# Performance work log

Hardware: AMD Instinct MI355X
Metric: run time of the kernel (lower is better)

The kernel has to match this reference:

```python
import jax, jax.numpy as jnp
import numpy as np

ALPHA, BETA, THRESH, T = 0.9, 0.8, 1.0, 10


def _heaviside(x):
    return (x > 0).astype(x.dtype)


def _conv(x, w, b, stride):
    y = jax.lax.conv_general_dilated(
        x, w, window_strides=(stride, stride), padding='VALID',
        dimension_numbers=('NCHW', 'OIHW', 'NCHW'))
    return jax.nn.relu(y + b[None, :, None, None])


def setup_inputs() -> dict:
    key = jax.random.key(0)
    ks = jax.random.split(key, 16)
    B = 128
    state = jax.random.uniform(ks[0], (B, 3, 224, 224), dtype=jnp.float32)
    history = jax.random.uniform(ks[1], (B, 90), dtype=jnp.float32)
    fc_in = 64 * 24 * 24 + 90  # 36954

    def w(k, shape, fan_in):
        return jax.random.normal(k, shape, dtype=jnp.float32) * (1.0 / np.sqrt(fan_in))

    return {
        'state': state, 'history': history,
        'cw1': w(ks[2], (32, 3, 8, 8), 3 * 8 * 8), 'cb1': jnp.zeros((32,), jnp.float32),
        'cw2': w(ks[3], (64, 32, 4, 4), 32 * 4 * 4), 'cb2': jnp.zeros((64,), jnp.float32),
        'cw3': w(ks[4], (64, 64, 3, 3), 64 * 3 * 3), 'cb3': jnp.zeros((64,), jnp.float32),
        'w1': w(ks[5], (128, fc_in), fc_in), 'b1': jnp.zeros((128,), jnp.float32),
        'w2': w(ks[6], (256, 128), 128), 'b2': jnp.zeros((256,), jnp.float32),
        'w3': w(ks[7], (9, 256), 256), 'b3': jnp.zeros((9,), jnp.float32),
    }


def reference(state, history, cw1, cb1, cw2, cb2, cw3, cb3, w1, b1, w2, b2, w3, b3):
    B = state.shape[0]
    f = _conv(state, cw1, cb1, 4)
    f = _conv(f, cw2, cb2, 2)
    f = _conv(f, cw3, cb3, 1)
    x = jnp.concatenate([f.reshape(B, -1), history], axis=1)  # (B, 36954)
    # encoding='constant' -> input (hence h1) is identical every timestep
    h1 = x @ w1.T + b1  # (B,128)

    def lif(h, mem, syn):
        new_syn = ALPHA * syn + h
        new_mem = BETA * mem + new_syn
        out = _heaviside(new_mem - THRESH)
        return out, new_mem - out * THRESH, new_syn

    z = lambda d: jnp.zeros((B, d), x.dtype)
    carry0 = (z(128), z(128), z(256), z(256), z(9), z(9), z(9))

    def step(carry, _):
        mem1, syn1, mem2, syn2, mem3, syn3, pot = carry
        spk1, mem1, syn1 = lif(h1, mem1, syn1)
        h2 = spk1 @ w2.T + b2
        spk2, mem2, syn2 = lif(h2, mem2, syn2)
        h3 = spk2 @ w3.T + b3
        syn3 = ALPHA * syn3 + h3
        mem3 = BETA * mem3 + syn3
        pot = pot + mem3
        return (mem1, syn1, mem2, syn2, mem3, syn3, pot), None

    carry, _ = jax.lax.scan(step, carry0, None, length=T)
    return carry[6] / T
```

## Files before the change

kernel.cpp:

```cpp
#include <hip/hip_runtime.h>

#define ALPHA 0.9f
#define BETA  0.8f
#define XS 36960

typedef _Float16 f16;
typedef _Float16 f16x8 __attribute__((ext_vector_type(8)));
typedef float f32x4 __attribute__((ext_vector_type(4)));
typedef unsigned int u32;

#define GLOAD_LDS16(gsrc, ldst)                                        \
  __builtin_amdgcn_global_load_lds(                                    \
      (const __attribute__((address_space(1))) void*)(gsrc),           \
      (__attribute__((address_space(3))) void*)(ldst), 16, 0, 0)

__device__ inline u32 hpair(u32 d0, u32 d1) {
#if __has_builtin(__builtin_amdgcn_perm)
  return __builtin_amdgcn_perm(d1, d0, 0x05040100u);
#else
  return (d0 & 0xffffu) | (d1 << 16);
#endif
}
__device__ inline u32 lpair(u32 d0, u32 d1) {
#if __has_builtin(__builtin_amdgcn_perm)
  return __builtin_amdgcn_perm(d1, d0, 0x07060302u);
#else
  return (d0 >> 16) | (d1 & 0xffff0000u);
#endif
}

__device__ inline u32 pack_hl(float v) {
  f16 h = (f16)v;
  f16 l = (f16)(v - (float)h);
  return (u32)__builtin_bit_cast(unsigned short, h) |
         ((u32)__builtin_bit_cast(unsigned short, l) << 16);
}


__global__ __launch_bounds__(256) void prep_weights_kernel(
    const float* __restrict__ cw1, const float* __restrict__ cw2,
    const float* __restrict__ cw3, const float* __restrict__ w2,
    f16* __restrict__ w1h, f16* __restrict__ w1l,
    f16* __restrict__ w2h, f16* __restrict__ w2l,
    f16* __restrict__ w3h, f16* __restrict__ w3l,
    float* __restrict__ w2q) {
  int i = blockIdx.x * 256 + threadIdx.x;
  if (i < 6144)  { float v = cw1[i]; f16 h = (f16)v; w1h[i] = h; w1l[i] = (f16)(v - (float)h); }
  if (i < 32768) { float v = cw2[i]; f16 h = (f16)v; w2h[i] = h; w2l[i] = (f16)(v - (float)h); }
  if (i < 49152) {
    int oc = i / 768, r = i % 768;
    int c = r / 12, rr = r % 12, kh = rr >> 2, kw = rr & 3;
    float v = (kw < 3) ? cw3[oc * 576 + c * 9 + kh * 3 + kw] : 0.f;
    f16 h = (f16)v; w3h[i] = h; w3l[i] = (f16)(v - (float)h);
  }
  if (i < 32768) {
    int j = i >> 7, k = i & 127;
    w2q[((k >> 2) * 256 + j) * 4 + (k & 3)] = w2[i];
  }
}

__global__ __launch_bounds__(256) void pad_w1_kernel(
    const float* __restrict__ w1, float* __restrict__ w1p) {
  int i = blockIdx.x * 256 + threadIdx.x;
  if (i < 128 * 18480) {
    int j = i / 18480, c = i - j * 18480;
    float2 v;
    if (c < 18477) v = *(const float2*)&w1[(size_t)j * 36954 + c * 2];
    else v = make_float2(0.f, 0.f);
    *(float2*)&w1p[(size_t)j * XS + c * 2] = v;
  }
}

__global__ __launch_bounds__(256) void conv1_kernel(
    const float* __restrict__ in, const f16* __restrict__ wh,
    const f16* __restrict__ wl, const float* __restrict__ bias,
    u32* __restrict__ out) {
  constexpr int K = 192, KCH = 6, OW = 55, OHW = 3025, NPB = 128;
  __shared__ __attribute__((aligned(16))) f16 Ah[2 * 512], Al[2 * 512];
  __shared__ __attribute__((aligned(16))) float Bf[8 * 512];

  const int n = blockIdx.y, pos0 = blockIdx.x * NPB;
  const int t = threadIdx.x;
  const int w = t >> 6, lane = t & 63, quad = lane >> 4, l16 = lane & 15;
  const float* __restrict__ inb = in + (size_t)n * 3 * 224 * 224;

  const int rq = (t >> 4) & 3;
  int base[2];
#pragma unroll
  for (int si = 0; si < 2; ++si) {
    int s = t + si * 256;
    int pos = pos0 + (s >> 6) * 16 + (s & 15);
    if (pos > OHW - 1) pos = OHW - 1;
    int oh = pos / OW, ow = pos - oh * OW;
    base[si] = oh * 4 * 224 + ow * 4;
  }
  const int am = (t >> 6) * 16 + (t & 15);
  const int ak = ((t >> 4) & 3) * 8;

  int posv[2];
#pragma unroll
  for (int ntl = 0; ntl < 2; ++ntl)
    posv[ntl] = pos0 + (w * 2 + ntl) * 16 + l16;

  f32x4 acc[2][2] = {};

  for (int kt = 0; kt < KCH; ++kt) {
    __syncthreads();
    if (t < 128) {
      *(f16x8*)&Ah[t * 8] = *(const f16x8*)&wh[am * K + kt * 32 + ak];
      *(f16x8*)&Al[t * 8] = *(const f16x8*)&wl[am * K + kt * 32 + ak];
    }
    {
      int r = kt * 4 + rq;
      int c = r >> 3, kh = r & 7;
      int rowoff = c * 50176 + kh * 224;
#pragma unroll
      for (int si = 0; si < 2; ++si)
#pragma unroll
        for (int half = 0; half < 2; ++half)
          GLOAD_LDS16(inb + rowoff + base[si] + half * 4,
                      &Bf[(si * 4 + w) * 512 + half * 256]);
    }
    __syncthreads();

    f16x8 ah0 = *(const f16x8*)&Ah[0 * 512 + lane * 8];
    f16x8 ah1 = *(const f16x8*)&Ah[1 * 512 + lane * 8];
    f16x8 al0 = *(const f16x8*)&Al[0 * 512 + lane * 8];
    f16x8 al1 = *(const f16x8*)&Al[1 * 512 + lane * 8];
    f16x8 bh[2], bl[2];
#pragma unroll
    for (int ntl = 0; ntl < 2; ++ntl) {
      const float* bp = &Bf[(w * 2 + ntl) * 512 + lane * 4];
      float4 v0 = *(const float4*)bp;
      float4 v1 = *(const float4*)(bp + 256);
      float vv[8] = {v0.x, v0.y, v0.z, v0.w, v1.x, v1.y, v1.z, v1.w};
#pragma unroll
      for (int e = 0; e < 8; ++e) {
        f16 h = (f16)vv[e];
        bh[ntl][e] = h;
        bl[ntl][e] = (f16)(vv[e] - (float)h);
      }
    }
    acc[0][0] = __builtin_amdgcn_mfma_f32_16x16x32_f16(ah0, bh[0], acc[0][0], 0, 0, 0);
    acc[0][0] = __builtin_amdgcn_mfma_f32_16x16x32_f16(ah0, bl[0], acc[0][0], 0, 0, 0);
    acc[0][0] = __builtin_amdgcn_mfma_f32_16x16x32_f16(al0, bh[0], acc[0][0], 0, 0, 0);
    acc[1][0] = __builtin_amdgcn_mfma_f32_16x16x32_f16(ah1, bh[0], acc[1][0], 0, 0, 0);
    acc[1][0] = __builtin_amdgcn_mfma_f32_16x16x32_f16(ah1, bl[0], acc[1][0], 0, 0, 0);
    acc[1][0] = __builtin_amdgcn_mfma_f32_16x16x32_f16(al1, bh[0], acc[1][0], 0, 0, 0);
    acc[0][1] = __builtin_amdgcn_mfma_f32_16x16x32_f16(ah0, bh[1], acc[0][1], 0, 0, 0);
    acc[0][1] = __builtin_amdgcn_mfma_f32_16x16x32_f16(ah0, bl[1], acc[0][1], 0, 0, 0);
    acc[0][1] = __builtin_amdgcn_mfma_f32_16x16x32_f16(al0, bh[1], acc[0][1], 0, 0, 0);
    acc[1][1] = __builtin_amdgcn_mfma_f32_16x16x32_f16(ah1, bh[1], acc[1][1], 0, 0, 0);
    acc[1][1] = __builtin_amdgcn_mfma_f32_16x16x32_f16(ah1, bl[1], acc[1][1], 0, 0, 0);
    acc[1][1] = __builtin_amdgcn_mfma_f32_16x16x32_f16(al1, bh[1], acc[1][1], 0, 0, 0);
  }

#pragma unroll
  for (int mtl = 0; mtl < 2; ++mtl)
#pragma unroll
    for (int ntl = 0; ntl < 2; ++ntl)
#pragma unroll
      for (int r = 0; r < 4; ++r) {
        int oc  = mtl * 16 + quad * 4 + r;
        int pos = posv[ntl];
        if (pos < OHW) {
          float v = acc[mtl][ntl][r] + bias[oc];
          v = v > 0.f ? v : 0.f;
          out[((size_t)n * 32 + oc) * OHW + pos] = pack_hl(v);
        }
      }
}

template<int IC, int KH, int KWP, int KWV, int S, int IH, int IW,
         int OW, int OHW, int OC, int NPB, bool OUT_X>
__global__ __launch_bounds__(256) void convhl_kernel(
    const u32* __restrict__ in, const f16* __restrict__ wh,
    const f16* __restrict__ wl, const float* __restrict__ bias,
    void* __restrict__ outv) {
  constexpr int K = IC * KH * KWP;
  constexpr int KCH = K / 32;
  __shared__ __attribute__((aligned(16))) f16 Ah[4 * 512], Al[4 * 512];
  __shared__ __attribute__((aligned(16))) u32 Bhl[2][256 * 4];

  const int n = blockIdx.y, pos0 = blockIdx.x * NPB;
  const int t = threadIdx.x;
  const int w = t >> 6, lane = t & 63, quad = lane >> 4, l16 = lane & 15;
  const int woc = w & 1, wpos = w >> 1;
  const u32* __restrict__ inb = in + (size_t)n * IC * IH * IW;

  int pos = pos0 + (t >> 6) * 16 + (t & 15);
  if (pos > OHW - 1) pos = OHW - 1;
  int oh = pos / OW, ow = pos - oh * OW;
  const int ohS = oh * S, owS = ow * S;
  const int rq = ((t >> 4) & 3) * 2;
  const int am = (t >> 6) * 16 + (t & 15);
  const int ak = ((t >> 4) & 3) * 8;

  int posv[2];
#pragma unroll
  for (int ntl = 0; ntl < 2; ++ntl)
    posv[ntl] = pos0 + (wpos * 2 + ntl) * 16 + l16;

  f32x4 acc[2][2] = {};

  for (int kt = 0; kt < KCH; ++kt) {
    __syncthreads();
    *(f16x8*)&Ah[t * 8] = *(const f16x8*)&wh[am * K + kt * 32 + ak];
    *(f16x8*)&Al[t * 8] = *(const f16x8*)&wl[am * K + kt * 32 + ak];
#pragma unroll
    for (int half = 0; half < 2; ++half) {
      int row = kt * 8 + rq + half;
      int c = row / KH, kh = row - c * KH;
      const u32* p = inb + ((size_t)c * IH + ohS + kh) * IW + owS;
      uint4 d;
      d.x = p[0]; d.y = p[1]; d.z = p[2];
      d.w = (KWV < KWP) ? 0u : p[3];
      *(uint4*)&Bhl[half][t * 4] = d;
    }
    __syncthreads();

    f16x8 ah0 = *(const f16x8*)&Ah[(woc * 2 + 0) * 512 + lane * 8];
    f16x8 ah1 = *(const f16x8*)&Ah[(woc * 2 + 1) * 512 + lane * 8];
    f16x8 al0 = *(const f16x8*)&Al[(woc * 2 + 0) * 512 + lane * 8];
    f16x8 al1 = *(const f16x8*)&Al[(woc * 2 + 1) * 512 + lane * 8];
    f16x8 bh[2], bl[2];
#pragma unroll
    for (int ntl = 0; ntl < 2; ++ntl) {
      int sl = ((wpos * 2 + ntl) * 64 + lane) * 4;
      uint4 q0 = *(const uint4*)&Bhl[0][sl];
      uint4 q1 = *(const uint4*)&Bhl[1][sl];
      uint4 hv, lv;
      hv.x = hpair(q0.x, q0.y); lv.x = lpair(q0.x, q0.y);
      hv.y = hpair(q0.z, q0.w); lv.y = lpair(q0.z, q0.w);
      hv.z = hpair(q1.x, q1.y); lv.z = lpair(q1.x, q1.y);
      hv.w = hpair(q1.z, q1.w); lv.w = lpair(q1.z, q1.w);
      bh[ntl] = __builtin_bit_cast(f16x8, hv);
      bl[ntl] = __builtin_bit_cast(f16x8, lv);
    }
    acc[0][0] = __builtin_amdgcn_mfma_f32_16x16x32_f16(ah0, bh[0], acc[0][0], 0, 0, 0);
    acc[0][0] = __builtin_amdgcn_mfma_f32_16x16x32_f16(ah0, bl[0], acc[0][0], 0, 0, 0);
    acc[0][0] = __builtin_amdgcn_mfma_f32_16x16x32_f16(al0, bh[0], acc[0][0], 0, 0, 0);
    acc[1][0] = __builtin_amdgcn_mfma_f32_16x16x32_f16(ah1, bh[0], acc[1][0], 0, 0, 0);
    acc[1][0] = __builtin_amdgcn_mfma_f32_16x16x32_f16(ah1, bl[0], acc[1][0], 0, 0, 0);
    acc[1][0] = __builtin_amdgcn_mfma_f32_16x16x32_f16(al1, bh[0], acc[1][0], 0, 0, 0);
    acc[0][1] = __builtin_amdgcn_mfma_f32_16x16x32_f16(ah0, bh[1], acc[0][1], 0, 0, 0);
    acc[0][1] = __builtin_amdgcn_mfma_f32_16x16x32_f16(ah0, bl[1], acc[0][1], 0, 0, 0);
    acc[0][1] = __builtin_amdgcn_mfma_f32_16x16x32_f16(al0, bh[1], acc[0][1], 0, 0, 0);
    acc[1][1] = __builtin_amdgcn_mfma_f32_16x16x32_f16(ah1, bh[1], acc[1][1], 0, 0, 0);
    acc[1][1] = __builtin_amdgcn_mfma_f32_16x16x32_f16(ah1, bl[1], acc[1][1], 0, 0, 0);
    acc[1][1] = __builtin_amdgcn_mfma_f32_16x16x32_f16(al1, bh[1], acc[1][1], 0, 0, 0);
  }

#pragma unroll
  for (int mtl = 0; mtl < 2; ++mtl)
#pragma unroll
    for (int ntl = 0; ntl < 2; ++ntl)
#pragma unroll
      for (int r = 0; r < 4; ++r) {
        int oc = (woc * 2 + mtl) * 16 + quad * 4 + r;
        int p2 = posv[ntl];
        if (p2 < OHW) {
          float v = acc[mtl][ntl][r] + bias[oc];
          v = v > 0.f ? v : 0.f;
          if constexpr (OUT_X)
            ((float*)outv)[(size_t)n * XS + oc * OHW + p2] = v;
          else
            ((u32*)outv)[((size_t)n * OC + oc) * OHW + p2] = pack_hl(v);
        }
      }
}

__global__ __launch_bounds__(256) void histpack_kernel(
    const float* __restrict__ h, float* __restrict__ x) {
  int i = blockIdx.x * 256 + threadIdx.x;
  if (i < 128 * 96) {
    int n = i / 96, k = i % 96;
    x[(size_t)n * XS + 36864 + k] = (k < 90) ? h[n * 90 + k] : 0.f;
  }
}

#define FC1_KT 289
__global__ __launch_bounds__(256) void fc1_kernel(
    const float* __restrict__ x, const float* __restrict__ w1p,
    float* __restrict__ P) {
  int kt = blockIdx.x;
  int t  = threadIdx.x;
  int bq = t & 15, jq = t >> 4;
  __shared__ float xs[128 * 36];
  __shared__ float wsm[128 * 36];
  float acc[8][8];
#pragma unroll
  for (int bb = 0; bb < 8; ++bb)
#pragma unroll
    for (int jj = 0; jj < 8; ++jj) acc[bb][jj] = 0.f;

  int cs = t & 7;
  int rs = t >> 3;
#pragma unroll 1
  for (int s = 0; s < 4; ++s) {
    int k0 = kt * 128 + s * 32;
    __syncthreads();
#pragma unroll
    for (int p = 0; p < 4; ++p) {
      int r = rs + p * 32;
      int gk = k0 + cs * 4;
      float4 xv, wv;
      if (gk < 36954) {
        xv = *(const float4*)&x[(size_t)r * XS + gk];
        wv = *(const float4*)&w1p[(size_t)r * XS + gk];
      } else {
        xv = make_float4(0.f, 0.f, 0.f, 0.f);
        wv = make_float4(0.f, 0.f, 0.f, 0.f);
      }
      *(float4*)&xs[r * 36 + cs * 4] = xv;
      *(float4*)&wsm[r * 36 + cs * 4] = wv;
    }
    __syncthreads();
#pragma unroll 1
    for (int kk = 0; kk < 32; kk += 4) {
      float4 xv[8], wv[8];
#pragma unroll
      for (int i = 0; i < 8; ++i)
        xv[i] = *(const float4*)&xs[(bq + 16 * i) * 36 + kk];
#pragma unroll
      for (int i = 0; i < 8; ++i)
        wv[i] = *(const float4*)&wsm[(jq + 16 * i) * 36 + kk];
#pragma unroll
      for (int bb = 0; bb < 8; ++bb)
#pragma unroll
        for (int jj = 0; jj < 8; ++jj) {
          acc[bb][jj] = fmaf(xv[bb].x, wv[jj].x, acc[bb][jj]);
          acc[bb][jj] = fmaf(xv[bb].y, wv[jj].y, acc[bb][jj]);
          acc[bb][jj] = fmaf(xv[bb].z, wv[jj].z, acc[bb][jj]);
          acc[bb][jj] = fmaf(xv[bb].w, wv[jj].w, acc[bb][jj]);
        }
    }
  }
  float* Pb = P + (size_t)kt * 16384;
#pragma unroll
  for (int bb = 0; bb < 8; ++bb)
#pragma unroll
    for (int jj = 0; jj < 8; ++jj)
      Pb[(bq + 16 * bb) * 128 + jq + 16 * jj] = acc[bb][jj];
}

__global__ __launch_bounds__(256) void reduce_p_kernel(
    const float* __restrict__ P, const float* __restrict__ b1,
    float* __restrict__ h1s) {
  int idx = blockIdx.x * 256 + threadIdx.x;
  int j = idx & 127;
  float a0 = 0.f, a1 = 0.f, a2 = 0.f, a3 = 0.f;
  int kt = 0;
#pragma unroll 2
  for (; kt + 3 < FC1_KT; kt += 4) {
    a0 += P[(size_t)(kt + 0) * 16384 + idx];
    a1 += P[(size_t)(kt + 1) * 16384 + idx];
    a2 += P[(size_t)(kt + 2) * 16384 + idx];
    a3 += P[(size_t)(kt + 3) * 16384 + idx];
  }
  for (; kt < FC1_KT; ++kt) a0 += P[(size_t)kt * 16384 + idx];
  h1s[idx] = ((a0 + a1) + (a2 + a3)) + b1[j];
}

__global__ __launch_bounds__(256, 1) void recur_kernel(
    const float* __restrict__ h1s,
    const float4* __restrict__ w2q,
    const float* __restrict__ b2,
    const float* __restrict__ w3,
    const float* __restrict__ b3,
    float* __restrict__ out) {
  int b = blockIdx.x;
  int t = threadIdx.x;
  __shared__ float spk1s[128];
  __shared__ float spk2s[256];
  __shared__ float w3s[9 * 256];
  __shared__ float part[9][16];
  float4 w2c[32];
#pragma unroll
  for (int k4 = 0; k4 < 32; ++k4) w2c[k4] = w2q[k4 * 256 + t];
  for (int i = t; i < 9 * 256; i += 256) w3s[i] = w3[i];
  float h1 = (t < 128) ? h1s[b * 128 + t] : 0.f;
  float mem1 = 0.f, syn1 = 0.f, mem2 = 0.f, syn2 = 0.f;
  float b2v = b2[t];
  float mem3 = 0.f, syn3 = 0.f, pot = 0.f;
  float b3v = (t < 9) ? b3[t] : 0.f;
  int j3 = t >> 4, p = t & 15;
  __syncthreads();

  for (int step = 0; step < 10; ++step) {
    if (t < 128) {
      syn1 = ALPHA * syn1 + h1;
      mem1 = BETA * mem1 + syn1;
      float s = (mem1 > 1.0f) ? 1.0f : 0.0f;
      mem1 -= s;
      spk1s[t] = s;
    }
    __syncthreads();
    float h2 = b2v;
#pragma unroll
    for (int k4 = 0; k4 < 32; ++k4) {
      float4 s = *(const float4*)&spk1s[k4 * 4];
      h2 = fmaf(s.x, w2c[k4].x, h2);
      h2 = fmaf(s.y, w2c[k4].y, h2);
      h2 = fmaf(s.z, w2c[k4].z, h2);
      h2 = fmaf(s.w, w2c[k4].w, h2);
    }
    syn2 = ALPHA * syn2 + h2;
    mem2 = BETA * mem2 + syn2;
    float s2 = (mem2 > 1.0f) ? 1.0f : 0.0f;
    mem2 -= s2;
    spk2s[t] = s2;
    __syncthreads();
    if (t < 144) {
      float a = 0.f;
      const float* wr = &w3s[j3 * 256 + p * 16];
      const float* sp = &spk2s[p * 16];
#pragma unroll
      for (int e = 0; e < 16; ++e) a = fmaf(sp[e], wr[e], a);
      part[j3][p] = a;
    }
    __syncthreads();
    if (t < 9) {
      float a = b3v;
#pragma unroll
      for (int p2 = 0; p2 < 16; ++p2) a += part[t][p2];
      syn3 = ALPHA * syn3 + a;
      mem3 = BETA * mem3 + syn3;
      pot += mem3;
    }
  }
  if (t < 9) out[b * 9 + t] = pot * 0.1f;
}

extern "C" void kernel_launch(void* const* d_in, const int* in_sizes, int n_in,
                              void* d_out, int out_size, void* d_ws, size_t ws_size,
                              hipStream_t stream) {
  const float* state   = (const float*)d_in[0];
  const float* history = (const float*)d_in[1];
  const float* cw1 = (const float*)d_in[2];
  const float* cb1 = (const float*)d_in[3];
  const float* cw2 = (const float*)d_in[4];
  const float* cb2 = (const float*)d_in[5];
  const float* cw3 = (const float*)d_in[6];
  const float* cb3 = (const float*)d_in[7];
  const float* w1  = (const float*)d_in[8];
  const float* b1  = (const float*)d_in[9];
  const float* w2  = (const float*)d_in[10];
  const float* b2  = (const float*)d_in[11];
  const float* w3  = (const float*)d_in[12];
  const float* b3  = (const float*)d_in[13];
  float* out = (float*)d_out;
  char* ws = (char*)d_ws;

  u32*   f1hl = (u32*)(ws + 0);
  float* xb   = (float*)(ws + 0);
  float* w1p  = (float*)(ws + 18923520);
  u32*   f2hl = (u32*)(ws + 49561600);
  float* P    = (float*)(ws + 49561600);
  f16* wf1h = (f16*)(ws + 71712768);
  f16* wf1l = (f16*)(ws + 71725056);
  f16* wf2h = (f16*)(ws + 71737344);
  f16* wf2l = (f16*)(ws + 71802880);
  f16* wf3h = (f16*)(ws + 71868416);
  f16* wf3l = (f16*)(ws + 71966720);
  float* w2q = (float*)(ws + 72065024);
  float* h1s = (float*)(ws + 72196096);

  prep_weights_kernel<<<192, 256, 0, stream>>>(cw1, cw2, cw3, w2,
                                               wf1h, wf1l, wf2h, wf2l,
                                               wf3h, wf3l, w2q);
  conv1_kernel<<<dim3(24, 128), 256, 0, stream>>>(state, wf1h, wf1l, cb1, f1hl);
  convhl_kernel<32, 4, 4, 4, 2, 55, 55, 26, 676, 64, 64, false>
      <<<dim3(11, 128), 256, 0, stream>>>(f1hl, wf2h, wf2l, cb2, (void*)f2hl);
  pad_w1_kernel<<<9240, 256, 0, stream>>>(w1, w1p);
  convhl_kernel<64, 3, 4, 3, 1, 26, 26, 24, 576, 64, 64, true>
      <<<dim3(9, 128), 256, 0, stream>>>(f2hl, wf3h, wf3l, cb3, (void*)xb);
  histpack_kernel<<<48, 256, 0, stream>>>(history, xb);
  fc1_kernel<<<FC1_KT, 256, 0, stream>>>(xb, w1p, P);
  reduce_p_kernel<<<64, 256, 0, stream>>>(P, b1, h1s);
  recur_kernel<<<128, 256, 0, stream>>>(h1s, (const float4*)w2q, b2, w3, b3, out);
}
```

Before: 351.6 us.

## Double-buffer conv1 input staging per wave and keep weights in registers

```diff
diff --git a/kernel.cpp b/kernel.cpp
--- a/kernel.cpp
+++ b/kernel.cpp
@@ -76,63 +76,52 @@
     const f16* __restrict__ wl, const float* __restrict__ bias,
     u32* __restrict__ out) {
   constexpr int K = 192, KCH = 6, OW = 55, OHW = 3025, NPB = 128;
-  __shared__ __attribute__((aligned(16))) f16 Ah[2 * 512], Al[2 * 512];
-  __shared__ __attribute__((aligned(16))) float Bf[8 * 512];
+  __shared__ __attribute__((aligned(16))) float Bf[4][2][2][2][256];
 
   const int n = blockIdx.y, pos0 = blockIdx.x * NPB;
   const int t = threadIdx.x;
   const int w = t >> 6, lane = t & 63, quad = lane >> 4, l16 = lane & 15;
   const float* __restrict__ inb = in + (size_t)n * 3 * 224 * 224;
 
-  const int rq = (t >> 4) & 3;
-  int base[2];
-#pragma unroll
-  for (int si = 0; si < 2; ++si) {
-    int s = t + si * 256;
-    int pos = pos0 + (s >> 6) * 16 + (s & 15);
+  f16x8 ahr[2][KCH], alr[2][KCH];
+#pragma unroll
+  for (int mtl = 0; mtl < 2; ++mtl)
+#pragma unroll
+    for (int kt = 0; kt < KCH; ++kt) {
+      ahr[mtl][kt] = *(const f16x8*)&wh[(mtl * 16 + l16) * K + kt * 32 + quad * 8];
+      alr[mtl][kt] = *(const f16x8*)&wl[(mtl * 16 + l16) * K + kt * 32 + quad * 8];
+    }
+
+  int posv[2];
+  const float* pb[2];
+#pragma unroll
+  for (int ntl = 0; ntl < 2; ++ntl) {
+    int pos = pos0 + (w * 2 + ntl) * 16 + l16;
+    posv[ntl] = pos;
     if (pos > OHW - 1) pos = OHW - 1;
     int oh = pos / OW, ow = pos - oh * OW;
-    base[si] = oh * 4 * 224 + ow * 4;
-  }
-  const int am = (t >> 6) * 16 + (t & 15);
-  const int ak = ((t >> 4) & 3) * 8;
-
-  int posv[2];
-#pragma unroll
-  for (int ntl = 0; ntl < 2; ++ntl)
-    posv[ntl] = pos0 + (w * 2 + ntl) * 16 + l16;
+    pb[ntl] = inb + oh * 4 * 224 + ow * 4;
+  }
 
   f32x4 acc[2][2] = {};
 
-  for (int kt = 0; kt < KCH; ++kt) {
-    __syncthreads();
-    if (t < 128) {
-      *(f16x8*)&Ah[t * 8] = *(const f16x8*)&wh[am * K + kt * 32 + ak];
-      *(f16x8*)&Al[t * 8] = *(const f16x8*)&wl[am * K + kt * 32 + ak];
-    }
-    {
-      int r = kt * 4 + rq;
-      int c = r >> 3, kh = r & 7;
-      int rowoff = c * 50176 + kh * 224;
-#pragma unroll
-      for (int si = 0; si < 2; ++si)
-#pragma unroll
-        for (int half = 0; half < 2; ++half)
-          GLOAD_LDS16(inb + rowoff + base[si] + half * 4,
-                      &Bf[(si * 4 + w) * 512 + half * 256]);
-    }
-    __syncthreads();
-
-    f16x8 ah0 = *(const f16x8*)&Ah[0 * 512 + lane * 8];
-    f16x8 ah1 = *(const f16x8*)&Ah[1 * 512 + lane * 8];
-    f16x8 al0 = *(const f16x8*)&Al[0 * 512 + lane * 8];
-    f16x8 al1 = *(const f16x8*)&Al[1 * 512 + lane * 8];
+  auto STAGE = [&](int kt, int buf) {
+    int r = kt * 4 + quad;
+    int rowoff = (r >> 3) * 50176 + (r & 7) * 224;
+#pragma unroll
+    for (int ntl = 0; ntl < 2; ++ntl) {
+      const float* src = pb[ntl] + rowoff;
+      GLOAD_LDS16(src,     &Bf[w][buf][ntl][0][0]);
+      GLOAD_LDS16(src + 4, &Bf[w][buf][ntl][1][0]);
+    }
+  };
+
+  auto COMPUTE = [&](int kt, int buf) {
     f16x8 bh[2], bl[2];
 #pragma unroll
     for (int ntl = 0; ntl < 2; ++ntl) {
-      const float* bp = &Bf[(w * 2 + ntl) * 512 + lane * 4];
-      float4 v0 = *(const float4*)bp;
-      float4 v1 = *(const float4*)(bp + 256);
+      float4 v0 = *(const float4*)&Bf[w][buf][ntl][0][lane * 4];
+      float4 v1 = *(const float4*)&Bf[w][buf][ntl][1][lane * 4];
       float vv[8] = {v0.x, v0.y, v0.z, v0.w, v1.x, v1.y, v1.z, v1.w};
 #pragma unroll
       for (int e = 0; e < 8; ++e) {
@@ -141,18 +130,31 @@
         bl[ntl][e] = (f16)(vv[e] - (float)h);
       }
     }
-    acc[0][0] = __builtin_amdgcn_mfma_f32_16x16x32_f16(ah0, bh[0], acc[0][0], 0, 0, 0);
-    acc[0][0] = __builtin_amdgcn_mfma_f32_16x16x32_f16(ah0, bl[0], acc[0][0], 0, 0, 0);
-    acc[0][0] = __builtin_amdgcn_mfma_f32_16x16x32_f16(al0, bh[0], acc[0][0], 0, 0, 0);
-    acc[1][0] = __builtin_amdgcn_mfma_f32_16x16x32_f16(ah1, bh[0], acc[1][0], 0, 0, 0);
-    acc[1][0] = __builtin_amdgcn_mfma_f32_16x16x32_f16(ah1, bl[0], acc[1][0], 0, 0, 0);
-    acc[1][0] = __builtin_amdgcn_mfma_f32_16x16x32_f16(al1, bh[0], acc[1][0], 0, 0, 0);
-    acc[0][1] = __builtin_amdgcn_mfma_f32_16x16x32_f16(ah0, bh[1], acc[0][1], 0, 0, 0);
-    acc[0][1] = __builtin_amdgcn_mfma_f32_16x16x32_f16(ah0, bl[1], acc[0][1], 0, 0, 0);
-    acc[0][1] = __builtin_amdgcn_mfma_f32_16x16x32_f16(al0, bh[1], acc[0][1], 0, 0, 0);
-    acc[1][1] = __builtin_amdgcn_mfma_f32_16x16x32_f16(ah1, bh[1], acc[1][1], 0, 0, 0);
-    acc[1][1] = __builtin_amdgcn_mfma_f32_16x16x32_f16(ah1, bl[1], acc[1][1], 0, 0, 0);
-    acc[1][1] = __builtin_amdgcn_mfma_f32_16x16x32_f16(al1, bh[1], acc[1][1], 0, 0, 0);
+    acc[0][0] = __builtin_amdgcn_mfma_f32_16x16x32_f16(ahr[0][kt], bh[0], acc[0][0], 0, 0, 0);
+    acc[0][0] = __builtin_amdgcn_mfma_f32_16x16x32_f16(ahr[0][kt], bl[0], acc[0][0], 0, 0, 0);
+    acc[0][0] = __builtin_amdgcn_mfma_f32_16x16x32_f16(alr[0][kt], bh[0], acc[0][0], 0, 0, 0);
+    acc[1][0] = __builtin_amdgcn_mfma_f32_16x16x32_f16(ahr[1][kt], bh[0], acc[1][0], 0, 0, 0);
+    acc[1][0] = __builtin_amdgcn_mfma_f32_16x16x32_f16(ahr[1][kt], bl[0], acc[1][0], 0, 0, 0);
+    acc[1][0] = __builtin_amdgcn_mfma_f32_16x16x32_f16(alr[1][kt], bh[0], acc[1][0], 0, 0, 0);
+    acc[0][1] = __builtin_amdgcn_mfma_f32_16x16x32_f16(ahr[0][kt], bh[1], acc[0][1], 0, 0, 0);
+    acc[0][1] = __builtin_amdgcn_mfma_f32_16x16x32_f16(ahr[0][kt], bl[1], acc[0][1], 0, 0, 0);
+    acc[0][1] = __builtin_amdgcn_mfma_f32_16x16x32_f16(alr[0][kt], bh[1], acc[0][1], 0, 0, 0);
+    acc[1][1] = __builtin_amdgcn_mfma_f32_16x16x32_f16(ahr[1][kt], bh[1], acc[1][1], 0, 0, 0);
+    acc[1][1] = __builtin_amdgcn_mfma_f32_16x16x32_f16(ahr[1][kt], bl[1], acc[1][1], 0, 0, 0);
+    acc[1][1] = __builtin_amdgcn_mfma_f32_16x16x32_f16(alr[1][kt], bh[1], acc[1][1], 0, 0, 0);
+  };
+
+  STAGE(0, 0);
+#pragma unroll
+  for (int kt = 0; kt < KCH; ++kt) {
+    if (kt < KCH - 1) {
+      STAGE(kt + 1, (kt + 1) & 1);
+      asm volatile("s_waitcnt vmcnt(4)" ::: "memory");
+    } else {
+      asm volatile("s_waitcnt vmcnt(0)" ::: "memory");
+    }
+    __builtin_amdgcn_sched_barrier(0);
+    COMPUTE(kt, kt & 1);
   }
 
 #pragma unroll
```

Result: slower. 371.1 us (+5.6%).

## Double-buffer conv B tiles, load weights directly to registers, widen reduce parallelism

Applied to the files above, without the earlier changes.

```diff
diff --git a/kernel.cpp b/kernel.cpp
--- a/kernel.cpp
+++ b/kernel.cpp
@@ -179,8 +179,7 @@
     void* __restrict__ outv) {
   constexpr int K = IC * KH * KWP;
   constexpr int KCH = K / 32;
-  __shared__ __attribute__((aligned(16))) f16 Ah[4 * 512], Al[4 * 512];
-  __shared__ __attribute__((aligned(16))) u32 Bhl[2][256 * 4];
+  __shared__ __attribute__((aligned(16))) u32 Bhl[2][2][256 * 4];
 
   const int n = blockIdx.y, pos0 = blockIdx.x * NPB;
   const int t = threadIdx.x;
@@ -193,8 +192,11 @@
   int oh = pos / OW, ow = pos - oh * OW;
   const int ohS = oh * S, owS = ow * S;
   const int rq = ((t >> 4) & 3) * 2;
-  const int am = (t >> 6) * 16 + (t & 15);
-  const int ak = ((t >> 4) & 3) * 8;
+
+  const f16* __restrict__ wh0 = wh + (size_t)((woc * 2 + 0) * 16 + l16) * K;
+  const f16* __restrict__ wh1 = wh + (size_t)((woc * 2 + 1) * 16 + l16) * K;
+  const f16* __restrict__ wl0 = wl + (size_t)((woc * 2 + 0) * 16 + l16) * K;
+  const f16* __restrict__ wl1 = wl + (size_t)((woc * 2 + 1) * 16 + l16) * K;
 
   int posv[2];
 #pragma unroll
@@ -203,10 +205,7 @@
 
   f32x4 acc[2][2] = {};
 
-  for (int kt = 0; kt < KCH; ++kt) {
-    __syncthreads();
-    *(f16x8*)&Ah[t * 8] = *(const f16x8*)&wh[am * K + kt * 32 + ak];
-    *(f16x8*)&Al[t * 8] = *(const f16x8*)&wl[am * K + kt * 32 + ak];
+  auto STAGEB = [&](int kt, int buf) {
 #pragma unroll
     for (int half = 0; half < 2; ++half) {
       int row = kt * 8 + rq + half;
@@ -215,20 +214,24 @@
       uint4 d;
       d.x = p[0]; d.y = p[1]; d.z = p[2];
       d.w = (KWV < KWP) ? 0u : p[3];
-      *(uint4*)&Bhl[half][t * 4] = d;
-    }
-    __syncthreads();
-
-    f16x8 ah0 = *(const f16x8*)&Ah[(woc * 2 + 0) * 512 + lane * 8];
-    f16x8 ah1 = *(const f16x8*)&Ah[(woc * 2 + 1) * 512 + lane * 8];
-    f16x8 al0 = *(const f16x8*)&Al[(woc * 2 + 0) * 512 + lane * 8];
-    f16x8 al1 = *(const f16x8*)&Al[(woc * 2 + 1) * 512 + lane * 8];
+      *(uint4*)&Bhl[buf][half][t * 4] = d;
+    }
+  };
+
+  auto LOADA = [&](int kt, f16x8& h0, f16x8& h1, f16x8& l0, f16x8& l1) {
+    h0 = *(const f16x8*)&wh0[kt * 32 + quad * 8];
+    h1 = *(const f16x8*)&wh1[kt * 32 + quad * 8];
+    l0 = *(const f16x8*)&wl0[kt * 32 + quad * 8];
+    l1 = *(const f16x8*)&wl1[kt * 32 + quad * 8];
+  };
+
+  auto COMPUTE = [&](f16x8 ah0, f16x8 ah1, f16x8 al0, f16x8 al1, int buf) {
     f16x8 bh[2], bl[2];
 #pragma unroll
     for (int ntl = 0; ntl < 2; ++ntl) {
       int sl = ((wpos * 2 + ntl) * 64 + lane) * 4;
-      uint4 q0 = *(const uint4*)&Bhl[0][sl];
-      uint4 q1 = *(const uint4*)&Bhl[1][sl];
+      uint4 q0 = *(const uint4*)&Bhl[buf][0][sl];
+      uint4 q1 = *(const uint4*)&Bhl[buf][1][sl];
       uint4 hv, lv;
       hv.x = hpair(q0.x, q0.y); lv.x = lpair(q0.x, q0.y);
       hv.y = hpair(q0.z, q0.w); lv.y = lpair(q0.z, q0.w);
@@ -249,6 +252,21 @@
     acc[1][1] = __builtin_amdgcn_mfma_f32_16x16x32_f16(ah1, bh[1], acc[1][1], 0, 0, 0);
     acc[1][1] = __builtin_amdgcn_mfma_f32_16x16x32_f16(ah1, bl[1], acc[1][1], 0, 0, 0);
     acc[1][1] = __builtin_amdgcn_mfma_f32_16x16x32_f16(al1, bh[1], acc[1][1], 0, 0, 0);
+  };
+
+  f16x8 A0h0, A0h1, A0l0, A0l1, A1h0, A1h1, A1l0, A1l1;
+  LOADA(0, A0h0, A0h1, A0l0, A0l1);
+
+#pragma unroll 1
+  for (int kt = 0; kt < KCH; kt += 2) {
+    STAGEB(kt, 0);
+    LOADA(kt + 1, A1h0, A1h1, A1l0, A1l1);
+    __syncthreads();
+    COMPUTE(A0h0, A0h1, A0l0, A0l1, 0);
+    STAGEB(kt + 1, 1);
+    if (kt + 2 < KCH) LOADA(kt + 2, A0h0, A0h1, A0l0, A0l1);
+    __syncthreads();
+    COMPUTE(A1h0, A1h1, A1l0, A1l1, 1);
   }
 
 #pragma unroll
@@ -344,14 +362,23 @@
       Pb[(bq + 16 * bb) * 128 + jq + 16 * jj] = acc[bb][jj];
 }
 
-__global__ __launch_bounds__(256) void reduce_p_kernel(
+__global__ __launch_bounds__(64) void reduce_p_kernel(
     const float* __restrict__ P, const float* __restrict__ b1,
     float* __restrict__ h1s) {
-  int idx = blockIdx.x * 256 + threadIdx.x;
+  int idx = blockIdx.x * 64 + threadIdx.x;
   int j = idx & 127;
   float a0 = 0.f, a1 = 0.f, a2 = 0.f, a3 = 0.f;
   int kt = 0;
-#pragma unroll 2
+  for (; kt + 31 < FC1_KT; kt += 32) {
+    float v[32];
+#pragma unroll
+    for (int q = 0; q < 32; ++q)
+      v[q] = P[(size_t)(kt + q) * 16384 + idx];
+#pragma unroll
+    for (int q = 0; q < 32; q += 4) {
+      a0 += v[q]; a1 += v[q + 1]; a2 += v[q + 2]; a3 += v[q + 3];
+    }
+  }
   for (; kt + 3 < FC1_KT; kt += 4) {
     a0 += P[(size_t)(kt + 0) * 16384 + idx];
     a1 += P[(size_t)(kt + 1) * 16384 + idx];
@@ -477,6 +504,6 @@
       <<<dim3(9, 128), 256, 0, stream>>>(f2hl, wf3h, wf3l, cb3, (void*)xb);
   histpack_kernel<<<48, 256, 0, stream>>>(history, xb);
   fc1_kernel<<<FC1_KT, 256, 0, stream>>>(xb, w1p, P);
-  reduce_p_kernel<<<64, 256, 0, stream>>>(P, b1, h1s);
+  reduce_p_kernel<<<256, 64, 0, stream>>>(P, b1, h1s);
   recur_kernel<<<128, 256, 0, stream>>>(h1s, (const float4*)w2q, b2, w3, b3, out);
 }
```

Result: slower. 397.9 us (+13.2%).
